# Kernel tuning notes

Hardware: AMD Instinct MI355X
Metric: run time of the kernel (lower is better)

The kernel has to match this reference:

```python
import jax, jax.numpy as jnp
import numpy as np

N = 100000      # nodes
E = 1600000     # edges (self-loops added in reference, as PyG GATConv does)
DIN = 512
DOUT = 16
H = 8           # heads (both layers)
C1 = 8          # out_channels of gat1
NEG_SLOPE = 0.2


def setup_inputs() -> dict:
    key = jax.random.key(0)
    ks = jax.random.split(key, 12)
    s = 0.05  # small init scale
    return {
        "x": jax.random.normal(ks[0], (N, DIN), jnp.float32),
        "edge_index": jax.random.randint(ks[1], (2, E), 0, N, jnp.int32),
        "W1": jax.random.normal(ks[2], (DIN, H * C1), jnp.float32) * s,
        "att_src1": jax.random.normal(ks[3], (H, C1), jnp.float32) * s,
        "att_dst1": jax.random.normal(ks[4], (H, C1), jnp.float32) * s,
        "bias1": jnp.zeros((H * C1,), jnp.float32),
        "prelu_w": jnp.float32(0.25),
        "W2": jax.random.normal(ks[5], (H * C1, H * DOUT), jnp.float32) * s,
        "att_src2": jax.random.normal(ks[6], (H, DOUT), jnp.float32) * s,
        "att_dst2": jax.random.normal(ks[7], (H, DOUT), jnp.float32) * s,
        "bias2": jnp.zeros((DOUT,), jnp.float32),
    }


def gat_layer(x, src, dst, W, a_src, a_dst, bias, heads, outc, concat):
    """PyG-style GATConv (eval mode, self-loops already in src/dst)."""
    n = x.shape[0]
    h = (x @ W).reshape(n, heads, outc)                 # [N, H, C]
    alpha_s = jnp.sum(h * a_src, axis=-1)               # [N, H]
    alpha_d = jnp.sum(h * a_dst, axis=-1)               # [N, H]
    # per-edge score, softmax grouped by destination node
    e = jax.nn.leaky_relu(alpha_s[src] + alpha_d[dst], NEG_SLOPE)   # [E', H]
    emax = jax.ops.segment_max(e, dst, num_segments=n)              # [N, H]
    ex = jnp.exp(e - emax[dst])
    denom = jax.ops.segment_sum(ex, dst, num_segments=n)            # [N, H]
    alpha = ex / denom[dst]                                         # [E', H]
    # weighted aggregation of source features
    out = jax.ops.segment_sum(h[src] * alpha[..., None], dst, num_segments=n)  # [N, H, C]
    out = out.reshape(n, heads * outc) if concat else out.mean(axis=1)
    return out + bias


def reference(x, edge_index, W1, att_src1, att_dst1, bias1, prelu_w,
              W2, att_src2, att_dst2, bias2):
    # add self-loops (PyG GATConv default add_self_loops=True)
    loops = jnp.arange(N, dtype=edge_index.dtype)
    src = jnp.concatenate([edge_index[0], loops])
    dst = jnp.concatenate([edge_index[1], loops])

    h = gat_layer(x, src, dst, W1, att_src1, att_dst1, bias1, H, C1, True)   # [N, 64]
    h = jnp.where(h >= 0, h, prelu_w * h)                                    # PReLU
    h = gat_layer(h, src, dst, W2, att_src2, att_dst2, bias2, H, DOUT, False)  # [N, DOUT]
    return jax.nn.log_softmax(h, axis=1)
```

## Files before the change

### kernel.cpp

```cpp
#include <hip/hip_runtime.h>
#include <hip/hip_bf16.h>

#define NN 100000
#define EE 1600000
#define ET (EE + NN)
#define NBK 391
#define NBLK 208
#define STAGE_CAP 4096

typedef unsigned short ushort_t;
typedef short short8 __attribute__((ext_vector_type(8)));
typedef float f32x4 __attribute__((ext_vector_type(4)));

static __device__ __forceinline__ float b2f(unsigned short u) {
    return __uint_as_float(((unsigned int)u) << 16);
}
static __device__ __forceinline__ unsigned short f2b(float f) {
    unsigned int x = __float_as_uint(f);
    return (unsigned short)((x + 0x7fffu + ((x >> 16) & 1u)) >> 16);
}

static __device__ void gemm1_body(const float* __restrict__ x,
                                  const ushort_t* __restrict__ w1t,
                                  ushort_t* __restrict__ h1,
                                  char* smem_, int row0, int tid) {
    ushort_t (*xs)[136] = (ushort_t (*)[136])smem_;
    const int wid = tid >> 6, lane = tid & 63;
    const int l15 = lane & 15, qq = lane >> 4;
    f32x4 acc[4];
#pragma unroll
    for (int i = 0; i < 4; ++i) acc[i] = (f32x4)0.f;
    for (int kc = 0; kc < 4; ++kc) {
        float4 f[8];
#pragma unroll
        for (int i = 0; i < 8; ++i) {
            int f4i = tid + 256 * i;
            int rr = f4i >> 5;
            int cc = f4i & 31;
            long gr = (long)min(row0 + rr, NN - 1);
            f[i] = *(const float4*)(x + gr * 512 + kc * 128 + cc * 4);
        }
        __syncthreads();
#pragma unroll
        for (int i = 0; i < 8; ++i) {
            int f4i = tid + 256 * i;
            int rr = f4i >> 5, cc = f4i & 31;
            uint2 uu;
            uu.x = ((unsigned)f2b(f[i].y) << 16) | f2b(f[i].x);
            uu.y = ((unsigned)f2b(f[i].w) << 16) | f2b(f[i].z);
            *(uint2*)&xs[rr][cc * 4] = uu;
        }
        __syncthreads();
#pragma unroll
        for (int ks = 0; ks < 4; ++ks) {
            short8 b = *(const short8*)(w1t + (size_t)(wid * 16 + l15) * 512 + kc * 128 + ks * 32 + qq * 8);
#pragma unroll
            for (int mt = 0; mt < 4; ++mt) {
                short8 a = *(const short8*)&xs[mt * 16 + l15][ks * 32 + qq * 8];
                acc[mt] = __builtin_amdgcn_mfma_f32_16x16x32_bf16(a, b, acc[mt], 0, 0, 0);
            }
        }
    }
#pragma unroll
    for (int mt = 0; mt < 4; ++mt) {
        int node = row0 + mt * 16 + qq * 4;
#pragma unroll
        for (int rr = 0; rr < 4; ++rr) {
            if (node + rr < NN)
                h1[(size_t)(node + rr) * 64 + wid * 16 + l15] = f2b(acc[mt][rr]);
        }
    }
}

__global__ __launch_bounds__(256) void kfuse0(const float* __restrict__ W1,
                                              const float* __restrict__ W2,
                                              ushort_t* __restrict__ W1T,
                                              ushort_t* __restrict__ W2T,
                                              const int* __restrict__ ei,
                                              int* __restrict__ bbcnt) {
    __shared__ int hist[NBK];
    const int t = threadIdx.x;
    if ((int)blockIdx.x < 160) {
        int tid = blockIdx.x * 256 + t;
        if (tid < 32768) {
            int k = tid >> 6, c = tid & 63;
            W1T[c * 512 + k] = f2b(W1[tid]);
        } else if (tid < 40960) {
            int q = tid - 32768;
            int k = q >> 7, c = q & 127;
            W2T[c * 64 + k] = f2b(W2[q]);
        }
    } else {
        const int blk = blockIdx.x - 160;
        for (int i = t; i < NBK; i += 256) hist[i] = 0;
        __syncthreads();
        const int e0 = blk * 8192;
#pragma unroll
        for (int i = 0; i < 32; ++i) {
            int e = e0 + t + 256 * i;
            if (e < ET) {
                int dst = (e < EE) ? ei[EE + e] : (e - EE);
                atomicAdd(&hist[dst >> 8], 1);
            }
        }
        __syncthreads();
        for (int i = t; i < NBK; i += 256) bbcnt[blk * NBK + i] = hist[i];
    }
}

__global__ __launch_bounds__(512) void kbscan(int* __restrict__ bbcnt,
                                              int* __restrict__ bbase) {
    __shared__ int tot[512];
    const int t = threadIdx.x;
    int total = 0;
    if (t < NBK) {
        int run = 0;
#pragma unroll 8
        for (int blk = 0; blk < NBLK; ++blk) {
            int idx = blk * NBK + t;
            int v = bbcnt[idx];
            bbcnt[idx] = run;
            run += v;
        }
        total = run;
    }
    tot[t] = total;
    __syncthreads();
    for (int off = 1; off < 512; off <<= 1) {
        int u = (t >= off) ? tot[t - off] : 0;
        __syncthreads();
        tot[t] += u;
        __syncthreads();
    }
    if (t < NBK) bbase[t] = tot[t] - total;
    if (t == 0) bbase[NBK] = ET;
}

__global__ __launch_bounds__(256) void kfuse1(const int* __restrict__ ei,
                                              const int* __restrict__ bbcnt,
                                              const int* __restrict__ bbase,
                                              unsigned* __restrict__ pairs,
                                              const float* __restrict__ x,
                                              const ushort_t* __restrict__ w1t,
                                              ushort_t* __restrict__ h1) {
    __shared__ __align__(16) char smem[17408];
    const int t = threadIdx.x;
    if ((int)blockIdx.x < NBLK) {
        int* cur = (int*)smem;
        const int blk = blockIdx.x;
        for (int i = t; i < NBK; i += 256) cur[i] = bbase[i] + bbcnt[blk * NBK + i];
        __syncthreads();
        const int e0 = blk * 8192;
#pragma unroll
        for (int i = 0; i < 32; ++i) {
            int e = e0 + t + 256 * i;
            if (e < ET) {
                int src, dst;
                if (e < EE) { src = ei[e]; dst = ei[EE + e]; } else { src = dst = e - EE; }
                int pos = atomicAdd(&cur[dst >> 8], 1);
                pairs[pos] = (unsigned)src | ((unsigned)(dst & 255) << 17);
            }
        }
    } else {
        gemm1_body(x, w1t, h1, smem, (blockIdx.x - NBLK) * 64, t);
    }
}

__global__ __launch_bounds__(256) void kfuse2(const int* __restrict__ bbase,
                                              const unsigned* __restrict__ pairs,
                                              int* __restrict__ rowp,
                                              int* __restrict__ srt,
                                              const float* __restrict__ x,
                                              const ushort_t* __restrict__ w1t,
                                              ushort_t* __restrict__ h1) {
    __shared__ __align__(16) char smem[19456];
    const int t = threadIdx.x;
    if ((int)blockIdx.x < NBK) {
        int* hist = (int*)smem;
        int* scn = hist + 256;
        int* cur = scn + 256;
        unsigned* stage = (unsigned*)(smem + 3072);
        const int b = blockIdx.x;
        const int j0 = bbase[b], j1 = bbase[b + 1];
        const int cnt = j1 - j0;
        hist[t] = 0;
        __syncthreads();
        for (int i = t; i < cnt; i += 256) {
            unsigned p = pairs[j0 + i];
            if (i < STAGE_CAP) stage[i] = p;
            atomicAdd(&hist[p >> 17], 1);
        }
        __syncthreads();
        const int h = hist[t];
        scn[t] = h;
        __syncthreads();
        for (int off = 1; off < 256; off <<= 1) {
            int u = (t >= off) ? scn[t - off] : 0;
            __syncthreads();
            scn[t] += u;
            __syncthreads();
        }
        const int pref = scn[t] - h;
        const int node = b * 256 + t;
        if (node < NN) rowp[node] = j0 + pref;
        if (b == 0 && t == 0) rowp[NN] = ET;
        cur[t] = pref;
        __syncthreads();
        for (int i = t; i < cnt; i += 256) {
            unsigned p = (i < STAGE_CAP) ? stage[i] : pairs[j0 + i];
            int l = (int)(p >> 17);
            int pos = atomicAdd(&cur[l], 1);
            srt[j0 + pos] = (int)(p & 0x1FFFFu);
        }
    } else {
        gemm1_body(x, w1t, h1, smem, (782 + (int)blockIdx.x - NBK) * 64, t);
    }
}

__global__ __launch_bounds__(256) void kagg1(const int* __restrict__ rowp,
                                             const int* __restrict__ srt,
                                             const ushort_t* __restrict__ h1,
                                             const float* __restrict__ aws,
                                             const float* __restrict__ awd,
                                             const float* __restrict__ b1,
                                             const float* __restrict__ pw,
                                             ushort_t* __restrict__ hin) {
    int tid = blockIdx.x * 256 + threadIdx.x;
    int n = tid >> 4;
    int sub = tid & 15;
    int h = sub >> 1, half = sub & 1;
    float as_w[8], ad_w[8];
#pragma unroll
    for (int c = 0; c < 8; ++c) { as_w[c] = aws[h * 8 + c]; ad_w[c] = awd[h * 8 + c]; }
    uint4 hd = *(const uint4*)(h1 + (size_t)n * 64 + h * 8);
    const ushort_t* hdp = (const ushort_t*)&hd;
    float ad = 0.f;
#pragma unroll
    for (int c = 0; c < 8; ++c) ad += b2f(hdp[c]) * ad_w[c];
    int j0 = rowp[n], j1 = rowp[n + 1];
    float num[8]; float den = 0.f;
#pragma unroll
    for (int c = 0; c < 8; ++c) num[c] = 0.f;
    int j = j0 + half;
    uint4 hv;
    if (j < j1) {
        int s = srt[j];
        hv = *(const uint4*)(h1 + (size_t)s * 64 + h * 8);
    }
    while (j < j1) {
        int jn = j + 2;
        uint4 hn;
        if (jn < j1) {
            int sn = srt[jn];
            hn = *(const uint4*)(h1 + (size_t)sn * 64 + h * 8);
        }
        const ushort_t* hp = (const ushort_t*)&hv;
        float va[8];
#pragma unroll
        for (int c = 0; c < 8; ++c) va[c] = b2f(hp[c]);
        float sc = ad;
#pragma unroll
        for (int c = 0; c < 8; ++c) sc += va[c] * as_w[c];
        sc = (sc >= 0.f) ? sc : 0.2f * sc;
        float w = __expf(sc);
        den += w;
#pragma unroll
        for (int c = 0; c < 8; ++c) num[c] += w * va[c];
        j = jn;
        hv = hn;
    }
#pragma unroll
    for (int c = 0; c < 8; ++c) num[c] += __shfl_xor(num[c], 1);
    den += __shfl_xor(den, 1);
    if (half == 0) {
        float inv = 1.f / den;
        float pwf = pw[0];
        ushort_t o[8];
#pragma unroll
        for (int c = 0; c < 8; ++c) {
            float v = num[c] * inv + b1[h * 8 + c];
            v = (v >= 0.f) ? v : pwf * v;
            o[c] = f2b(v);
        }
        *(uint4*)(hin + (size_t)n * 64 + h * 8) = *(uint4*)o;
    }
}

__global__ __launch_bounds__(256) void kgemm2(const ushort_t* __restrict__ hin,
                                              const ushort_t* __restrict__ w2t,
                                              ushort_t* __restrict__ h2) {
    __shared__ __align__(16) ushort_t xs[64][72];
    const int tid = threadIdx.x;
    const int wid = tid >> 6, lane = tid & 63;
    const int l15 = lane & 15, qq = lane >> 4;
    const int row0 = blockIdx.x * 64;
    const int r = tid >> 2, seg = tid & 3;
    const long grow = (long)min(row0 + r, NN - 1);
    const uint4* gp = (const uint4*)(hin + grow * 64 + seg * 16);
    uint4 v0 = gp[0], v1 = gp[1];
    uint4* lp = (uint4*)&xs[r][seg * 16];
    lp[0] = v0; lp[1] = v1;
    __syncthreads();
    f32x4 acc[4][2];
#pragma unroll
    for (int i = 0; i < 4; ++i)
#pragma unroll
        for (int j = 0; j < 2; ++j) acc[i][j] = (f32x4)0.f;
#pragma unroll
    for (int ks = 0; ks < 2; ++ks) {
        short8 a[4];
#pragma unroll
        for (int mt = 0; mt < 4; ++mt)
            a[mt] = *(const short8*)&xs[mt * 16 + l15][ks * 32 + qq * 8];
#pragma unroll
        for (int nt = 0; nt < 2; ++nt) {
            short8 b = *(const short8*)(w2t + (size_t)(wid * 32 + nt * 16 + l15) * 64 + ks * 32 + qq * 8);
#pragma unroll
            for (int mt = 0; mt < 4; ++mt)
                acc[mt][nt] = __builtin_amdgcn_mfma_f32_16x16x32_bf16(a[mt], b, acc[mt][nt], 0, 0, 0);
        }
    }
#pragma unroll
    for (int mt = 0; mt < 4; ++mt) {
        int node = row0 + mt * 16 + qq * 4;
#pragma unroll
        for (int nt = 0; nt < 2; ++nt) {
            int col = wid * 32 + nt * 16 + l15;
#pragma unroll
            for (int rr = 0; rr < 4; ++rr) {
                if (node + rr < NN)
                    h2[(size_t)(node + rr) * 128 + col] = f2b(acc[mt][nt][rr]);
            }
        }
    }
}

__global__ __launch_bounds__(256) void kagg2(const int* __restrict__ rowp,
                                             const int* __restrict__ srt,
                                             const ushort_t* __restrict__ h2,
                                             const float* __restrict__ aws,
                                             const float* __restrict__ awd,
                                             const float* __restrict__ b2,
                                             float* __restrict__ out) {
    int tid = blockIdx.x * 256 + threadIdx.x;
    int n = tid >> 4;
    int sub = tid & 15;
    int h = sub >> 1, half = sub & 1;
    float as_w[16], ad_w[16];
#pragma unroll
    for (int c = 0; c < 16; ++c) { as_w[c] = aws[h * 16 + c]; ad_w[c] = awd[h * 16 + c]; }
    uint4 d0 = *(const uint4*)(h2 + (size_t)n * 128 + h * 16);
    uint4 d1 = *(const uint4*)(h2 + (size_t)n * 128 + h * 16 + 8);
    const ushort_t* dp0 = (const ushort_t*)&d0;
    const ushort_t* dp1 = (const ushort_t*)&d1;
    float ad = 0.f;
#pragma unroll
    for (int c = 0; c < 8; ++c) { ad += b2f(dp0[c]) * ad_w[c]; ad += b2f(dp1[c]) * ad_w[8 + c]; }
    int j0 = rowp[n], j1 = rowp[n + 1];
    float num[16]; float den = 0.f;
#pragma unroll
    for (int c = 0; c < 16; ++c) num[c] = 0.f;
    int j = j0 + half;
    uint4 v0, v1;
    if (j < j1) {
        int s = srt[j];
        const uint4* rp = (const uint4*)(h2 + (size_t)s * 128 + h * 16);
        v0 = rp[0]; v1 = rp[1];
    }
    while (j < j1) {
        int jn = j + 2;
        uint4 n0, n1;
        if (jn < j1) {
            int sn = srt[jn];
            const uint4* rp = (const uint4*)(h2 + (size_t)sn * 128 + h * 16);
            n0 = rp[0]; n1 = rp[1];
        }
        const ushort_t* p0 = (const ushort_t*)&v0;
        const ushort_t* p1 = (const ushort_t*)&v1;
        float va[16];
#pragma unroll
        for (int c = 0; c < 8; ++c) { va[c] = b2f(p0[c]); va[8 + c] = b2f(p1[c]); }
        float sc = ad;
#pragma unroll
        for (int c = 0; c < 16; ++c) sc += va[c] * as_w[c];
        sc = (sc >= 0.f) ? sc : 0.2f * sc;
        float w = __expf(sc);
        den += w;
#pragma unroll
        for (int c = 0; c < 16; ++c) num[c] += w * va[c];
        j = jn;
        v0 = n0; v1 = n1;
    }
#pragma unroll
    for (int c = 0; c < 16; ++c) num[c] += __shfl_xor(num[c], 1);
    den += __shfl_xor(den, 1);
    float sden = 0.125f / den;
    float v[16];
#pragma unroll
    for (int c = 0; c < 16; ++c) v[c] = num[c] * sden;
#pragma unroll
    for (int mask = 2; mask <= 8; mask <<= 1)
#pragma unroll
        for (int c = 0; c < 16; ++c) v[c] += __shfl_xor(v[c], mask);
#pragma unroll
    for (int c = 0; c < 16; ++c) v[c] += b2[c];
    float m = v[0];
#pragma unroll
    for (int c = 1; c < 16; ++c) m = fmaxf(m, v[c]);
    float sum = 0.f;
#pragma unroll
    for (int c = 0; c < 16; ++c) sum += __expf(v[c] - m);
    float ls = __logf(sum) + m;
    out[(size_t)n * 16 + sub] = v[sub] - ls;
}

extern "C" void kernel_launch(void* const* d_in, const int* in_sizes, int n_in,
                              void* d_out, int out_size, void* d_ws, size_t ws_size,
                              hipStream_t stream) {
    const float* x    = (const float*)d_in[0];
    const int*   ei   = (const int*)d_in[1];
    const float* W1   = (const float*)d_in[2];
    const float* aws1 = (const float*)d_in[3];
    const float* awd1 = (const float*)d_in[4];
    const float* b1   = (const float*)d_in[5];
    const float* pw   = (const float*)d_in[6];
    const float* W2   = (const float*)d_in[7];
    const float* aws2 = (const float*)d_in[8];
    const float* awd2 = (const float*)d_in[9];
    const float* b2   = (const float*)d_in[10];
    float* out = (float*)d_out;

    char* ws = (char*)d_ws;
    int*      srt   = (int*)(ws + 0);
    int*      rowp  = (int*)(ws + 6800000);
    int*      bbcnt = (int*)(ws + 7200256);
    int*      bbase = (int*)(ws + 7600384);
    unsigned* pairs = (unsigned*)(ws + 8000000);
    ushort_t* hin   = (ushort_t*)(ws + 8000000);
    ushort_t* h1    = (ushort_t*)(ws + 20800000);
    ushort_t* h2    = (ushort_t*)(ws + 20800000);
    ushort_t* W1T   = (ushort_t*)(ws + 46400000);
    ushort_t* W2T   = (ushort_t*)(ws + 46465536);

    kfuse0<<<160 + NBLK, 256, 0, stream>>>(W1, W2, W1T, W2T, ei, bbcnt);
    kbscan<<<1, 512, 0, stream>>>(bbcnt, bbase);
    kfuse1<<<NBLK + 782, 256, 0, stream>>>(ei, bbcnt, bbase, pairs, x, W1T, h1);
    kfuse2<<<NBK + 781, 256, 0, stream>>>(bbase, pairs, rowp, srt, x, W1T, h1);
    kagg1<<<6250, 256, 0, stream>>>(rowp, srt, h1, aws1, awd1, b1, pw, hin);
    kgemm2<<<1563, 256, 0, stream>>>(hin, W2T, h2);
    kagg2<<<6250, 256, 0, stream>>>(rowp, srt, h2, aws2, awd2, b2, out);
}
```

Baseline: 502.5 us.

## Aggregate layer-2 on 64-wide inputs before projecting with W2

Layer 2 no longer materialises the 128-wide h2. Attention logits are computed from hin using folded vectors W2·a_src and W2·a_dst, precomputed in the first kernel. Each node's 64-wide inputs are aggregated per head with the softmax weights, and a per-block MFMA then projects the result through W2, ending with a fused head-mean and log_softmax. This removes the gemm2 kernel, the h2 write/read traffic and the per-edge 16-wide dot products, at the cost of a 32-float accumulator per thread, a serial per-thread edge loop, and an extra bf16 rounding of the aggregates.

```diff
diff --git a/kernel.cpp b/kernel.cpp
--- a/kernel.cpp
+++ b/kernel.cpp
@@ -7,6 +7,8 @@
 #define NBK 391
 #define NBLK 208
 #define STAGE_CAP 4096
+#define AGG_NS 72
+#define AGG_HS 1160
 
 typedef unsigned short ushort_t;
 typedef short short8 __attribute__((ext_vector_type(8)));
@@ -77,7 +79,10 @@
                                               ushort_t* __restrict__ W1T,
                                               ushort_t* __restrict__ W2T,
                                               const int* __restrict__ ei,
-                                              int* __restrict__ bbcnt) {
+                                              int* __restrict__ bbcnt,
+                                              const float* __restrict__ aws2,
+                                              const float* __restrict__ awd2,
+                                              float* __restrict__ qp) {
     __shared__ int hist[NBK];
     const int t = threadIdx.x;
     if ((int)blockIdx.x < 160) {
@@ -90,7 +95,7 @@
             int k = q >> 7, c = q & 127;
             W2T[c * 64 + k] = f2b(W2[q]);
         }
-    } else {
+    } else if ((int)blockIdx.x < 368) {
         const int blk = blockIdx.x - 160;
         for (int i = t; i < NBK; i += 256) hist[i] = 0;
         __syncthreads();
@@ -105,6 +110,16 @@
         }
         __syncthreads();
         for (int i = t; i < NBK; i += 256) bbcnt[blk * NBK + i] = hist[i];
+    } else {
+        for (int e = t; e < 1024; e += 256) {
+            int base = (e >= 512) ? (e - 512) : e;
+            int h = base >> 6, k = base & 63;
+            const float* w = (e >= 512) ? awd2 : aws2;
+            float val = 0.f;
+#pragma unroll
+            for (int c = 0; c < 16; ++c) val += W2[k * 128 + h * 16 + c] * w[h * 16 + c];
+            qp[e] = val;
+        }
     }
 }
 
@@ -286,132 +301,140 @@
     }
 }
 
-__global__ __launch_bounds__(256) void kgemm2(const ushort_t* __restrict__ hin,
+__global__ __launch_bounds__(256) void kalpha2f(const ushort_t* __restrict__ hin,
+                                                const float* __restrict__ qp,
+                                                float* __restrict__ as2,
+                                                float* __restrict__ ad2) {
+    __shared__ float lq[1024];
+    const int t = threadIdx.x;
+    for (int i = t; i < 1024; i += 256) lq[i] = qp[i];
+    __syncthreads();
+    int gid = blockIdx.x * 256 + t;
+    int n = gid >> 3, h = gid & 7;
+    float s = 0.f, d = 0.f;
+#pragma unroll
+    for (int g = 0; g < 8; ++g) {
+        uint4 v = *(const uint4*)(hin + (size_t)n * 64 + g * 8);
+        const ushort_t* p = (const ushort_t*)&v;
+        float4 qa = *(const float4*)&lq[h * 64 + g * 8];
+        float4 qb = *(const float4*)&lq[h * 64 + g * 8 + 4];
+        float4 pa = *(const float4*)&lq[512 + h * 64 + g * 8];
+        float4 pb = *(const float4*)&lq[512 + h * 64 + g * 8 + 4];
+        s += b2f(p[0]) * qa.x + b2f(p[1]) * qa.y + b2f(p[2]) * qa.z + b2f(p[3]) * qa.w;
+        s += b2f(p[4]) * qb.x + b2f(p[5]) * qb.y + b2f(p[6]) * qb.z + b2f(p[7]) * qb.w;
+        d += b2f(p[0]) * pa.x + b2f(p[1]) * pa.y + b2f(p[2]) * pa.z + b2f(p[3]) * pa.w;
+        d += b2f(p[4]) * pb.x + b2f(p[5]) * pb.y + b2f(p[6]) * pb.z + b2f(p[7]) * pb.w;
+    }
+    as2[gid] = s;
+    ad2[gid] = d;
+}
+
+__global__ __launch_bounds__(256) void kagg2f(const int* __restrict__ rowp,
+                                              const int* __restrict__ srt,
+                                              const ushort_t* __restrict__ hin,
+                                              const float* __restrict__ as2,
+                                              const float* __restrict__ ad2,
                                               const ushort_t* __restrict__ w2t,
-                                              ushort_t* __restrict__ h2) {
-    __shared__ __align__(16) ushort_t xs[64][72];
-    const int tid = threadIdx.x;
-    const int wid = tid >> 6, lane = tid & 63;
-    const int l15 = lane & 15, qq = lane >> 4;
-    const int row0 = blockIdx.x * 64;
-    const int r = tid >> 2, seg = tid & 3;
-    const long grow = (long)min(row0 + r, NN - 1);
-    const uint4* gp = (const uint4*)(hin + grow * 64 + seg * 16);
-    uint4 v0 = gp[0], v1 = gp[1];
-    uint4* lp = (uint4*)&xs[r][seg * 16];
-    lp[0] = v0; lp[1] = v1;
-    __syncthreads();
-    f32x4 acc[4][2];
-#pragma unroll
-    for (int i = 0; i < 4; ++i)
-#pragma unroll
-        for (int j = 0; j < 2; ++j) acc[i][j] = (f32x4)0.f;
-#pragma unroll
-    for (int ks = 0; ks < 2; ++ks) {
-        short8 a[4];
-#pragma unroll
-        for (int mt = 0; mt < 4; ++mt)
-            a[mt] = *(const short8*)&xs[mt * 16 + l15][ks * 32 + qq * 8];
-#pragma unroll
-        for (int nt = 0; nt < 2; ++nt) {
-            short8 b = *(const short8*)(w2t + (size_t)(wid * 32 + nt * 16 + l15) * 64 + ks * 32 + qq * 8);
-#pragma unroll
-            for (int mt = 0; mt < 4; ++mt)
-                acc[mt][nt] = __builtin_amdgcn_mfma_f32_16x16x32_bf16(a[mt], b, acc[mt][nt], 0, 0, 0);
-        }
-    }
-#pragma unroll
-    for (int mt = 0; mt < 4; ++mt) {
-        int node = row0 + mt * 16 + qq * 4;
-#pragma unroll
-        for (int nt = 0; nt < 2; ++nt) {
-            int col = wid * 32 + nt * 16 + l15;
-#pragma unroll
-            for (int rr = 0; rr < 4; ++rr) {
-                if (node + rr < NN)
-                    h2[(size_t)(node + rr) * 128 + col] = f2b(acc[mt][nt][rr]);
-            }
-        }
-    }
-}
-
-__global__ __launch_bounds__(256) void kagg2(const int* __restrict__ rowp,
-                                             const int* __restrict__ srt,
-                                             const ushort_t* __restrict__ h2,
-                                             const float* __restrict__ aws,
-                                             const float* __restrict__ awd,
-                                             const float* __restrict__ b2,
-                                             float* __restrict__ out) {
-    int tid = blockIdx.x * 256 + threadIdx.x;
-    int n = tid >> 4;
-    int sub = tid & 15;
-    int h = sub >> 1, half = sub & 1;
-    float as_w[16], ad_w[16];
-#pragma unroll
-    for (int c = 0; c < 16; ++c) { as_w[c] = aws[h * 16 + c]; ad_w[c] = awd[h * 16 + c]; }
-    uint4 d0 = *(const uint4*)(h2 + (size_t)n * 128 + h * 16);
-    uint4 d1 = *(const uint4*)(h2 + (size_t)n * 128 + h * 16 + 8);
-    const ushort_t* dp0 = (const ushort_t*)&d0;
-    const ushort_t* dp1 = (const ushort_t*)&d1;
-    float ad = 0.f;
-#pragma unroll
-    for (int c = 0; c < 8; ++c) { ad += b2f(dp0[c]) * ad_w[c]; ad += b2f(dp1[c]) * ad_w[8 + c]; }
-    int j0 = rowp[n], j1 = rowp[n + 1];
-    float num[16]; float den = 0.f;
-#pragma unroll
-    for (int c = 0; c < 16; ++c) num[c] = 0.f;
-    int j = j0 + half;
-    uint4 v0, v1;
-    if (j < j1) {
-        int s = srt[j];
-        const uint4* rp = (const uint4*)(h2 + (size_t)s * 128 + h * 16);
-        v0 = rp[0]; v1 = rp[1];
-    }
+                                              const float* __restrict__ b2,
+                                              float* __restrict__ out) {
+    __shared__ __align__(16) ushort_t agg[8 * AGG_HS];
+    __shared__ float red[4][16][16];
+    const int t = threadIdx.x;
+    const int nl = t >> 4, sub = t & 15;
+    const int h = sub >> 1, half = sub & 1;
+    const int n = blockIdx.x * 16 + nl;
+    const float ad = ad2[n * 8 + h];
+    const int j0 = rowp[n], j1 = rowp[n + 1];
+    float num[32];
+#pragma unroll
+    for (int c = 0; c < 32; ++c) num[c] = 0.f;
+    float den = 0.f;
+    int j = j0;
+    int s0 = srt[j];
+    float as_ = as2[s0 * 8 + h];
+    const ushort_t* rp = hin + (size_t)s0 * 64 + half * 32;
+    uint4 r0 = *(const uint4*)(rp);
+    uint4 r1 = *(const uint4*)(rp + 8);
+    uint4 r2 = *(const uint4*)(rp + 16);
+    uint4 r3 = *(const uint4*)(rp + 24);
     while (j < j1) {
-        int jn = j + 2;
-        uint4 n0, n1;
+        int jn = j + 1;
+        uint4 n0, n1, n2, n3;
+        float asn = 0.f;
         if (jn < j1) {
             int sn = srt[jn];
-            const uint4* rp = (const uint4*)(h2 + (size_t)sn * 128 + h * 16);
-            n0 = rp[0]; n1 = rp[1];
-        }
-        const ushort_t* p0 = (const ushort_t*)&v0;
-        const ushort_t* p1 = (const ushort_t*)&v1;
-        float va[16];
-#pragma unroll
-        for (int c = 0; c < 8; ++c) { va[c] = b2f(p0[c]); va[8 + c] = b2f(p1[c]); }
-        float sc = ad;
-#pragma unroll
-        for (int c = 0; c < 16; ++c) sc += va[c] * as_w[c];
+            asn = as2[sn * 8 + h];
+            const ushort_t* np = hin + (size_t)sn * 64 + half * 32;
+            n0 = *(const uint4*)(np);
+            n1 = *(const uint4*)(np + 8);
+            n2 = *(const uint4*)(np + 16);
+            n3 = *(const uint4*)(np + 24);
+        }
+        float sc = as_ + ad;
         sc = (sc >= 0.f) ? sc : 0.2f * sc;
         float w = __expf(sc);
         den += w;
-#pragma unroll
-        for (int c = 0; c < 16; ++c) num[c] += w * va[c];
+        {
+            const ushort_t* p = (const ushort_t*)&r0;
+#pragma unroll
+            for (int c = 0; c < 8; ++c) num[c] += w * b2f(p[c]);
+        }
+        {
+            const ushort_t* p = (const ushort_t*)&r1;
+#pragma unroll
+            for (int c = 0; c < 8; ++c) num[8 + c] += w * b2f(p[c]);
+        }
+        {
+            const ushort_t* p = (const ushort_t*)&r2;
+#pragma unroll
+            for (int c = 0; c < 8; ++c) num[16 + c] += w * b2f(p[c]);
+        }
+        {
+            const ushort_t* p = (const ushort_t*)&r3;
+#pragma unroll
+            for (int c = 0; c < 8; ++c) num[24 + c] += w * b2f(p[c]);
+        }
         j = jn;
-        v0 = n0; v1 = n1;
-    }
-#pragma unroll
-    for (int c = 0; c < 16; ++c) num[c] += __shfl_xor(num[c], 1);
-    den += __shfl_xor(den, 1);
-    float sden = 0.125f / den;
-    float v[16];
-#pragma unroll
-    for (int c = 0; c < 16; ++c) v[c] = num[c] * sden;
-#pragma unroll
-    for (int mask = 2; mask <= 8; mask <<= 1)
-#pragma unroll
-        for (int c = 0; c < 16; ++c) v[c] += __shfl_xor(v[c], mask);
-#pragma unroll
-    for (int c = 0; c < 16; ++c) v[c] += b2[c];
-    float m = v[0];
-#pragma unroll
-    for (int c = 1; c < 16; ++c) m = fmaxf(m, v[c]);
-    float sum = 0.f;
-#pragma unroll
-    for (int c = 0; c < 16; ++c) sum += __expf(v[c] - m);
-    float ls = __logf(sum) + m;
-    out[(size_t)n * 16 + sub] = v[sub] - ls;
+        r0 = n0; r1 = n1; r2 = n2; r3 = n3;
+        as_ = asn;
+    }
+    float g = 0.125f / den;
+#pragma unroll
+    for (int q = 0; q < 4; ++q) {
+        ushort_t o[8];
+#pragma unroll
+        for (int c = 0; c < 8; ++c) o[c] = f2b(num[q * 8 + c] * g);
+        *(uint4*)&agg[h * AGG_HS + nl * AGG_NS + half * 32 + q * 8] = *(uint4*)o;
+    }
+    __syncthreads();
+    const int wid = t >> 6, lane = t & 63;
+    const int l15 = lane & 15, qq = lane >> 4;
+    f32x4 acc = (f32x4)0.f;
+#pragma unroll
+    for (int hh2 = 0; hh2 < 2; ++hh2) {
+        int hh = wid + hh2 * 4;
+#pragma unroll
+        for (int ks = 0; ks < 2; ++ks) {
+            short8 a = *(const short8*)&agg[hh * AGG_HS + l15 * AGG_NS + ks * 32 + qq * 8];
+            short8 b = *(const short8*)(w2t + (size_t)(hh * 16 + l15) * 64 + ks * 32 + qq * 8);
+            acc = __builtin_amdgcn_mfma_f32_16x16x32_bf16(a, b, acc, 0, 0, 0);
+        }
+    }
+#pragma unroll
+    for (int r = 0; r < 4; ++r) red[wid][qq * 4 + r][l15] = acc[r];
+    __syncthreads();
+    {
+        int c = sub;
+        float v = red[0][nl][c] + red[1][nl][c] + red[2][nl][c] + red[3][nl][c] + b2[c];
+        float m = v;
+#pragma unroll
+        for (int mask = 1; mask <= 8; mask <<= 1) m = fmaxf(m, __shfl_xor(m, mask));
+        float e = __expf(v - m);
+        float sum = e;
+#pragma unroll
+        for (int mask = 1; mask <= 8; mask <<= 1) sum += __shfl_xor(sum, mask);
+        out[(size_t)n * 16 + c] = v - (__logf(sum) + m);
+    }
 }
 
 extern "C" void kernel_launch(void* const* d_in, const int* in_sizes, int n_in,
@@ -438,15 +461,17 @@
     unsigned* pairs = (unsigned*)(ws + 8000000);
     ushort_t* hin   = (ushort_t*)(ws + 8000000);
     ushort_t* h1    = (ushort_t*)(ws + 20800000);
-    ushort_t* h2    = (ushort_t*)(ws + 20800000);
+    float*    as2   = (float*)(ws + 20800000);
+    float*    ad2   = (float*)(ws + 24000000);
     ushort_t* W1T   = (ushort_t*)(ws + 46400000);
     ushort_t* W2T   = (ushort_t*)(ws + 46465536);
-
-    kfuse0<<<160 + NBLK, 256, 0, stream>>>(W1, W2, W1T, W2T, ei, bbcnt);
+    float*    qp    = (float*)(ws + 46481920);
+
+    kfuse0<<<369, 256, 0, stream>>>(W1, W2, W1T, W2T, ei, bbcnt, aws2, awd2, qp);
     kbscan<<<1, 512, 0, stream>>>(bbcnt, bbase);
     kfuse1<<<NBLK + 782, 256, 0, stream>>>(ei, bbcnt, bbase, pairs, x, W1T, h1);
     kfuse2<<<NBK + 781, 256, 0, stream>>>(bbase, pairs, rowp, srt, x, W1T, h1);
     kagg1<<<6250, 256, 0, stream>>>(rowp, srt, h1, aws1, awd1, b1, pw, hin);
-    kgemm2<<<1563, 256, 0, stream>>>(hin, W2T, h2);
-    kagg2<<<6250, 256, 0, stream>>>(rowp, srt, h2, aws2, awd2, b2, out);
-}
+    kalpha2f<<<3125, 256, 0, stream>>>(hin, qp, as2, ad2);
+    kagg2f<<<6250, 256, 0, stream>>>(rowp, srt, hin, as2, ad2, W2T, b2, out);
+}
```

Measured after the change: 576.8 us. 14.8% more time.
